# Optimization experiments

Measured on AMD Instinct MI355X. Metric: run time of the kernel, lower is better.

## Reference

```python
import jax, jax.numpy as jnp
import numpy as np

D_MODEL = 1024
NUM_HEADS = 16
D_K = D_MODEL // NUM_HEADS


def setup_inputs() -> dict:
    key = jax.random.key(0)
    ks = jax.random.split(key, 11)
    s = 1.0 / np.sqrt(D_MODEL)
    return {
        "Q": jax.random.normal(ks[0], (2, 2048, D_MODEL), jnp.float32),
        "K": jax.random.normal(ks[1], (2, 2048, D_MODEL), jnp.float32),
        "V": jax.random.normal(ks[2], (2, 2048, D_MODEL), jnp.float32),
        "W_Q": jax.random.uniform(ks[3], (D_MODEL, D_MODEL), jnp.float32, -s, s),
        "b_Q": jax.random.uniform(ks[4], (D_MODEL,), jnp.float32, -s, s),
        "W_K": jax.random.uniform(ks[5], (D_K, D_MODEL), jnp.float32, -s, s),
        "b_K": jax.random.uniform(ks[6], (D_K,), jnp.float32, -s, s),
        "W_V": jax.random.uniform(ks[7], (D_K, D_MODEL), jnp.float32, -s, s),
        "b_V": jax.random.uniform(ks[8], (D_K,), jnp.float32, -s, s),
        "W_O": jax.random.uniform(ks[9], (D_MODEL, D_MODEL), jnp.float32, -s, s),
        "b_O": jax.random.uniform(ks[10], (D_MODEL,), jnp.float32, -s, s),
    }


def reference(Q, K, V, W_Q, b_Q, W_K, b_K, W_V, b_V, W_O, b_O):
    B, S, _ = Q.shape
    # Q projection -> [B, H, S, d_k]
    q = (Q @ W_Q.T + b_Q).reshape(B, S, NUM_HEADS, D_K).transpose(0, 2, 1, 3)
    # shared single-head K/V -> [B, S, d_k] (broadcast across heads)
    k = K @ W_K.T + b_K
    v = V @ W_V.T + b_V
    scale = 1.0 / jnp.sqrt(jnp.asarray(D_K, q.dtype))
    scores = jnp.einsum('bhqd,bkd->bhqk', q, k) * scale  # [B,H,S,S]
    attn = jax.nn.softmax(scores, axis=-1)
    out = jnp.einsum('bhqk,bkd->bhqd', attn, v)  # [B,H,S,d_k]
    out = out.transpose(0, 2, 1, 3).reshape(B, S, D_MODEL)
    return out @ W_O.T + b_O
```

## Files before the change

### kernel.cpp

```cpp
#include <hip/hip_runtime.h>
#include <hip/hip_bf16.h>
#include <math.h>

#define D_MODEL 1024
#define NUM_HEADS 16
#define DK 64
#define BATCH 2
#define SEQ 2048
#define MROWS (BATCH * SEQ)

#define QSCALE (0.125f * 1.4426950408889634f)

typedef __attribute__((ext_vector_type(8))) short bf16x8;
typedef __attribute__((ext_vector_type(4))) float f32x4;

static __device__ __forceinline__ short f2bf(float f) {
    __hip_bfloat16 h = __float2bfloat16(f);
    union { __hip_bfloat16 h; short s; } c; c.h = h; return c.s;
}

static __device__ __forceinline__ unsigned pkbf2(float a, float b) {
    __hip_bfloat162 h = __float22bfloat162_rn(make_float2(a, b));
    union { __hip_bfloat162 h; unsigned u; } c; c.h = h; return c.u;
}

static __device__ __forceinline__ void gload16(const void* g, void* l) {
    __builtin_amdgcn_global_load_lds(
        (const __attribute__((address_space(1))) unsigned int*)g,
        (__attribute__((address_space(3))) unsigned int*)l, 16, 0, 0);
}

__global__ __launch_bounds__(256) void cvt6(
    const float* __restrict__ q, const float* __restrict__ k,
    const float* __restrict__ v, const float* __restrict__ wq,
    const float* __restrict__ wo, const float* __restrict__ wk,
    const float* __restrict__ wv,
    short* __restrict__ qo, short* __restrict__ ko, short* __restrict__ vo,
    short* __restrict__ wqo, short* __restrict__ woo, short* __restrict__ wko,
    short* __restrict__ wvo)
{
    const int NB = (MROWS * D_MODEL) / 8;
    const int NW = (D_MODEL * D_MODEL) / 8;
    const int NS = (DK * D_MODEL) / 8;
    const int total = 3 * NB + 2 * NW + 2 * NS;
    for (int g = blockIdx.x * 256 + threadIdx.x; g < total; g += gridDim.x * 256) {
        const float* s; short* d; int x = g;
        if (x < NB)            { s = q;  d = qo;  }
        else if ((x -= NB) < NB) { s = k;  d = ko;  }
        else if ((x -= NB) < NB) { s = v;  d = vo;  }
        else if ((x -= NB) < NW) { s = wq; d = wqo; }
        else if ((x -= NW) < NW) { s = wo; d = woo; }
        else if ((x -= NW) < NS) { s = wk; d = wko; }
        else                     { x -= NS; s = wv; d = wvo; }
        float4 a = ((const float4*)s)[x * 2];
        float4 b = ((const float4*)s)[x * 2 + 1];
        uint4 hv;
        hv.x = pkbf2(a.x, a.y); hv.y = pkbf2(a.z, a.w);
        hv.z = pkbf2(b.x, b.y); hv.w = pkbf2(b.z, b.w);
        ((uint4*)d)[x] = hv;
    }
}

template<int MODE, int BM, int BN>
__global__ __launch_bounds__(256) void gemm97(
    const short* __restrict__ A, const short* __restrict__ W,
    const float* __restrict__ bias, void* __restrict__ Cp,
    const short* __restrict__ A2, const short* __restrict__ W2,
    const float* __restrict__ bias2, void* __restrict__ Cp2,
    int M, int N, int K, float outmult)
{
    constexpr int MI = BM / 32;
    constexpr int NI = BN / 32;
    constexpr int ACH = BM / 32;
    constexpr int WCH = BN / 32;
    __shared__ short As[BM * 64];
    __shared__ short Ws[BN * 64];

    int sel = 0;
    if (MODE == 2) {
        sel = blockIdx.y;
        if (sel) { A = A2; W = W2; bias = bias2; Cp = Cp2; }
    }
    const int bm = blockIdx.x * BM;
    const int bn = (MODE == 2) ? 0 : blockIdx.y * BN;
    const int tid = threadIdx.x;
    const int l = tid & 63, w = tid >> 6;
    const int lr = l & 15, lg = l >> 4;
    const int wm = (w >> 1) * (BM / 2), wn = (w & 1) * (BN / 2);

    f32x4 acc[MI][NI];
    #pragma unroll
    for (int mi = 0; mi < MI; mi++)
        #pragma unroll
        for (int ni = 0; ni < NI; ni++)
            acc[mi][ni] = (f32x4){0.f, 0.f, 0.f, 0.f};

    const int srow = l >> 3;
    const int scol = (l & 7) * 8;

    for (int k0 = 0; k0 < K; k0 += 64) {
        __syncthreads();
        #pragma unroll
        for (int i = 0; i < ACH; i++) {
            int c = w * ACH + i;
            gload16(A + (size_t)(bm + 8 * c + srow) * K + k0 + scol, As + c * 512);
        }
        #pragma unroll
        for (int i = 0; i < WCH; i++) {
            int c = w * WCH + i;
            gload16(W + (size_t)(bn + 8 * c + srow) * K + k0 + scol, Ws + c * 512);
        }
        __syncthreads();
        #pragma unroll
        for (int ks = 0; ks < 2; ks++) {
            bf16x8 af[MI], bf[NI];
            #pragma unroll
            for (int mi = 0; mi < MI; mi++)
                af[mi] = *(const bf16x8*)&As[(wm + mi * 16 + lr) * 64 + ks * 32 + 8 * lg];
            #pragma unroll
            for (int ni = 0; ni < NI; ni++)
                bf[ni] = *(const bf16x8*)&Ws[(wn + ni * 16 + lr) * 64 + ks * 32 + 8 * lg];
            #pragma unroll
            for (int mi = 0; mi < MI; mi++)
                #pragma unroll
                for (int ni = 0; ni < NI; ni++)
                    acc[mi][ni] = __builtin_amdgcn_mfma_f32_16x16x32_bf16(
                        af[mi], bf[ni], acc[mi][ni], 0, 0, 0);
        }
    }

    #pragma unroll
    for (int ni = 0; ni < NI; ni++) {
        int col = bn + wn + ni * 16 + lr;
        float bv = bias[col];
        #pragma unroll
        for (int mi = 0; mi < MI; mi++) {
            #pragma unroll
            for (int r = 0; r < 4; r++) {
                int row = bm + wm + mi * 16 + lg * 4 + r;
                float val = (acc[mi][ni][r] + bv) * outmult;
                if (MODE == 0) {
                    ((short*)Cp)[(size_t)row * N + col] = f2bf(val);
                } else if (MODE == 1) {
                    ((float*)Cp)[(size_t)row * N + col] = val;
                } else {
                    if (sel == 0) {
                        ((short*)Cp)[(size_t)row * DK + col] = f2bf(val);
                    } else {
                        int bi = row >> 11, si = row & (SEQ - 1);
                        ((short*)Cp)[((size_t)bi * DK + col) * SEQ + si] = f2bf(val);
                    }
                }
            }
        }
    }
}

__global__ __launch_bounds__(256, 3) void mqa_attn_lds(
    const short* __restrict__ qb, const short* __restrict__ kb,
    const short* __restrict__ vt, short* __restrict__ ob)
{
    __shared__ char KsB[2][64 * 128];
    __shared__ char VsB[2][64 * 128];
    __shared__ char Ps[4][32 * 128];
    const int h = blockIdx.y, b = blockIdx.z;
    const int tid = threadIdx.x;
    const int l = tid & 63, w = tid >> 6;
    const int lr = l & 15, lg = l >> 4;
    const int q0 = blockIdx.x * 128 + w * 32;
    char* myPs = Ps[w];

    bf16x8 qf[2][2];
    #pragma unroll
    for (int qt = 0; qt < 2; qt++)
        #pragma unroll
        for (int kk = 0; kk < 2; kk++)
            qf[qt][kk] = *(const bf16x8*)(
                qb + (size_t)(b * SEQ + q0 + qt * 16 + lr) * D_MODEL + h * DK + kk * 32 + 8 * lg);

    int srow[2], scol[2];
    #pragma unroll
    for (int i = 0; i < 2; i++) {
        int s = i * 256 + w * 64 + l;
        srow[i] = s >> 3;
        int cb = (s & 7) * 16;
        scol[i] = (cb ^ ((srow[i] & 7) << 4)) >> 1;
    }

    f32x4 o[4][2];
    #pragma unroll
    for (int dt = 0; dt < 4; dt++)
        #pragma unroll
        for (int qt = 0; qt < 2; qt++)
            o[dt][qt] = (f32x4){0.f, 0.f, 0.f, 0.f};
    float m_i[2] = {-1e30f, -1e30f};
    float l_i[2] = {0.f, 0.f};

    #pragma unroll
    for (int i = 0; i < 2; i++) {
        gload16(kb + (size_t)(b * SEQ + 0 + srow[i]) * DK + scol[i],
                KsB[0] + (i * 256 + w * 64) * 16);
        gload16(vt + (size_t)(b * DK + srow[i]) * SEQ + 0 + scol[i],
                VsB[0] + (i * 256 + w * 64) * 16);
    }

    for (int t = 0; t < SEQ / 64; t++) {
        const int cur = t & 1;
        const int kt = t * 64;
        __syncthreads();
        if (t + 1 < SEQ / 64) {
            const int ktn = kt + 64;
            #pragma unroll
            for (int i = 0; i < 2; i++) {
                gload16(kb + (size_t)(b * SEQ + ktn + srow[i]) * DK + scol[i],
                        KsB[cur ^ 1] + (i * 256 + w * 64) * 16);
                gload16(vt + (size_t)(b * DK + srow[i]) * SEQ + ktn + scol[i],
                        VsB[cur ^ 1] + (i * 256 + w * 64) * 16);
            }
        }
        const char* Kc = KsB[cur];
        const char* Vc = VsB[cur];

        f32x4 s[2][4];
        #pragma unroll
        for (int qt = 0; qt < 2; qt++)
            #pragma unroll
            for (int j = 0; j < 4; j++) s[qt][j] = (f32x4){0.f, 0.f, 0.f, 0.f};
        #pragma unroll
        for (int kk = 0; kk < 2; kk++) {
            bf16x8 kf[4];
            #pragma unroll
            for (int j = 0; j < 4; j++) {
                int row = j * 16 + lr;
                kf[j] = *(const bf16x8*)(Kc + row * 128 + ((kk * 64 + 16 * lg) ^ ((row & 7) << 4)));
            }
            __builtin_amdgcn_s_setprio(1);
            #pragma unroll
            for (int qt = 0; qt < 2; qt++)
                #pragma unroll
                for (int j = 0; j < 4; j++)
                    s[qt][j] = __builtin_amdgcn_mfma_f32_16x16x32_bf16(
                        kf[j], qf[qt][kk], s[qt][j], 0, 0, 0);
            __builtin_amdgcn_s_setprio(0);
        }

        float corr[2]; int resc[2];
        #pragma unroll
        for (int qt = 0; qt < 2; qt++) {
            float mA = fmaxf(fmaxf(s[qt][0][0], s[qt][0][1]), s[qt][0][2]);
            float mB = fmaxf(fmaxf(s[qt][0][3], s[qt][1][0]), s[qt][1][1]);
            float mC = fmaxf(fmaxf(s[qt][1][2], s[qt][1][3]), s[qt][2][0]);
            float mD = fmaxf(fmaxf(s[qt][2][1], s[qt][2][2]), s[qt][2][3]);
            float mE = fmaxf(fmaxf(s[qt][3][0], s[qt][3][1]), s[qt][3][2]);
            float mx = fmaxf(fmaxf(fmaxf(mA, mB), mC),
                             fmaxf(fmaxf(mD, mE), s[qt][3][3]));
            mx = fmaxf(mx, __shfl_xor(mx, 16));
            mx = fmaxf(mx, __shfl_xor(mx, 32));

            resc[qt] = __any(mx > m_i[qt] + 8.0f);
            if (resc[qt]) {
                float mn = fmaxf(m_i[qt], mx);
                corr[qt] = __builtin_amdgcn_exp2f(m_i[qt] - mn);
                m_i[qt] = mn;
            } else {
                corr[qt] = 1.0f;
            }
            const float mnv = m_i[qt];

            float rs = 0.f;
            const int row = qt * 16 + lr;
            char* base = myPs + row * 128;
            const int sw = (row & 7) << 4;
            #pragma unroll
            for (int j = 0; j < 4; j++) {
                float p0 = __builtin_amdgcn_exp2f(s[qt][j][0] - mnv);
                float p1 = __builtin_amdgcn_exp2f(s[qt][j][1] - mnv);
                float p2 = __builtin_amdgcn_exp2f(s[qt][j][2] - mnv);
                float p3 = __builtin_amdgcn_exp2f(s[qt][j][3] - mnv);
                rs += (p0 + p1) + (p2 + p3);
                uint2 pk;
                pk.x = pkbf2(p0, p1);
                pk.y = pkbf2(p2, p3);
                *(uint2*)(base + ((j * 32 + lg * 8) ^ sw)) = pk;
            }
            rs += __shfl_xor(rs, 16);
            rs += __shfl_xor(rs, 32);
            l_i[qt] = l_i[qt] * corr[qt] + rs;
        }
        #pragma unroll
        for (int qt = 0; qt < 2; qt++)
            if (resc[qt]) {
                #pragma unroll
                for (int dt = 0; dt < 4; dt++)
                    o[dt][qt] *= corr[qt];
            }

        #pragma unroll
        for (int kk = 0; kk < 2; kk++) {
            bf16x8 vf[4], pf[2];
            #pragma unroll
            for (int dt = 0; dt < 4; dt++) {
                int row = dt * 16 + lr;
                vf[dt] = *(const bf16x8*)(Vc + row * 128 + ((kk * 64 + 16 * lg) ^ ((row & 7) << 4)));
            }
            #pragma unroll
            for (int qt = 0; qt < 2; qt++) {
                int row = qt * 16 + lr;
                pf[qt] = *(bf16x8*)(myPs + row * 128 + ((kk * 64 + 16 * lg) ^ ((row & 7) << 4)));
            }
            __builtin_amdgcn_s_setprio(1);
            #pragma unroll
            for (int dt = 0; dt < 4; dt++)
                #pragma unroll
                for (int qt = 0; qt < 2; qt++)
                    o[dt][qt] = __builtin_amdgcn_mfma_f32_16x16x32_bf16(
                        vf[dt], pf[qt], o[dt][qt], 0, 0, 0);
            __builtin_amdgcn_s_setprio(0);
        }
    }

    #pragma unroll
    for (int qt = 0; qt < 2; qt++) {
        float inv = 1.0f / l_i[qt];
        size_t grow = (size_t)(b * SEQ + q0 + qt * 16 + lr);
        #pragma unroll
        for (int dt = 0; dt < 4; dt++) {
            uint2 pk;
            pk.x = pkbf2(o[dt][qt][0] * inv, o[dt][qt][1] * inv);
            pk.y = pkbf2(o[dt][qt][2] * inv, o[dt][qt][3] * inv);
            *(uint2*)(ob + grow * D_MODEL + h * DK + dt * 16 + lg * 4) = pk;
        }
    }
}

extern "C" void kernel_launch(void* const* d_in, const int* in_sizes, int n_in,
                              void* d_out, int out_size, void* d_ws, size_t ws_size,
                              hipStream_t stream) {
    const float* Q   = (const float*)d_in[0];
    const float* K   = (const float*)d_in[1];
    const float* V   = (const float*)d_in[2];
    const float* W_Q = (const float*)d_in[3];
    const float* b_Q = (const float*)d_in[4];
    const float* W_K = (const float*)d_in[5];
    const float* b_K = (const float*)d_in[6];
    const float* W_V = (const float*)d_in[7];
    const float* b_V = (const float*)d_in[8];
    const float* W_O = (const float*)d_in[9];
    const float* b_O = (const float*)d_in[10];
    float* out = (float*)d_out;

    short* Qb  = (short*)d_ws;
    short* Kb  = Qb  + (size_t)MROWS * D_MODEL;
    short* Vb  = Kb  + (size_t)MROWS * D_MODEL;
    short* WQb = Vb  + (size_t)MROWS * D_MODEL;
    short* WKb = WQb + (size_t)D_MODEL * D_MODEL;
    short* WVb = WKb + (size_t)DK * D_MODEL;
    short* WOb = WVb + (size_t)DK * D_MODEL;
    short* qb  = WOb + (size_t)D_MODEL * D_MODEL;
    short* kb  = qb  + (size_t)MROWS * D_MODEL;
    short* vt  = kb  + (size_t)MROWS * DK;
    short* aws = vt  + (size_t)MROWS * DK;

    cvt6<<<2048, 256, 0, stream>>>(Q, K, V, W_Q, W_O, W_K, W_V,
                                   Qb, Kb, Vb, WQb, WOb, WKb, WVb);

    gemm97<0, 64, 128><<<dim3(MROWS / 64, D_MODEL / 128), 256, 0, stream>>>(
        Qb, WQb, b_Q, qb, nullptr, nullptr, nullptr, nullptr,
        MROWS, D_MODEL, D_MODEL, QSCALE);
    gemm97<2, 64, 64><<<dim3(MROWS / 64, 2), 256, 0, stream>>>(
        Kb, WKb, b_K, kb, Vb, WVb, b_V, vt, MROWS, DK, D_MODEL, 1.0f);
    mqa_attn_lds<<<dim3(SEQ / 128, NUM_HEADS, BATCH), 256, 0, stream>>>(
        qb, kb, vt, aws);
    gemm97<1, 64, 128><<<dim3(MROWS / 64, D_MODEL / 128), 256, 0, stream>>>(
        aws, WOb, b_O, out, nullptr, nullptr, nullptr, nullptr,
        MROWS, D_MODEL, D_MODEL, 1.0f);
}
```

Measured before the change: 132.5 us.

## Halve attention query tile per wave and defer row-sum reduction

The attention kernel now gives each wave 16 query rows instead of 32, so each block covers 64 queries, the grid doubles, and launch bounds rise to 4 blocks per CU with a smaller P buffer in LDS. The per-row sum reduction across lanes moves out of the KV loop and runs once at the end, and the max shuffle only runs when a rescale is triggered. The aim is more waves and occupancy with fewer cross-lane ops per iteration, at the cost of reloading each K/V tile from global memory for twice as many blocks and lower MFMA reuse per K/V fragment.

```diff
diff --git a/kernel.cpp b/kernel.cpp
--- a/kernel.cpp
+++ b/kernel.cpp
@@ -156,27 +156,25 @@
     }
 }
 
-__global__ __launch_bounds__(256, 3) void mqa_attn_lds(
+__global__ __launch_bounds__(256, 4) void mqa_attn_lds(
     const short* __restrict__ qb, const short* __restrict__ kb,
     const short* __restrict__ vt, short* __restrict__ ob)
 {
     __shared__ char KsB[2][64 * 128];
     __shared__ char VsB[2][64 * 128];
-    __shared__ char Ps[4][32 * 128];
+    __shared__ char Ps[4][16 * 128];
     const int h = blockIdx.y, b = blockIdx.z;
     const int tid = threadIdx.x;
     const int l = tid & 63, w = tid >> 6;
     const int lr = l & 15, lg = l >> 4;
-    const int q0 = blockIdx.x * 128 + w * 32;
+    const int q0 = blockIdx.x * 64 + w * 16;
     char* myPs = Ps[w];
 
-    bf16x8 qf[2][2];
-    #pragma unroll
-    for (int qt = 0; qt < 2; qt++)
-        #pragma unroll
-        for (int kk = 0; kk < 2; kk++)
-            qf[qt][kk] = *(const bf16x8*)(
-                qb + (size_t)(b * SEQ + q0 + qt * 16 + lr) * D_MODEL + h * DK + kk * 32 + 8 * lg);
+    bf16x8 qf[2];
+    #pragma unroll
+    for (int kk = 0; kk < 2; kk++)
+        qf[kk] = *(const bf16x8*)(
+            qb + (size_t)(b * SEQ + q0 + lr) * D_MODEL + h * DK + kk * 32 + 8 * lg);
 
     int srow[2], scol[2];
     #pragma unroll
@@ -187,14 +185,12 @@
         scol[i] = (cb ^ ((srow[i] & 7) << 4)) >> 1;
     }
 
-    f32x4 o[4][2];
+    f32x4 o[4];
     #pragma unroll
     for (int dt = 0; dt < 4; dt++)
-        #pragma unroll
-        for (int qt = 0; qt < 2; qt++)
-            o[dt][qt] = (f32x4){0.f, 0.f, 0.f, 0.f};
-    float m_i[2] = {-1e30f, -1e30f};
-    float l_i[2] = {0.f, 0.f};
+        o[dt] = (f32x4){0.f, 0.f, 0.f, 0.f};
+    float m_i = -1e30f;
+    float l_l = 0.f;
 
     #pragma unroll
     for (int i = 0; i < 2; i++) {
@@ -221,11 +217,9 @@
         const char* Kc = KsB[cur];
         const char* Vc = VsB[cur];
 
-        f32x4 s[2][4];
-        #pragma unroll
-        for (int qt = 0; qt < 2; qt++)
-            #pragma unroll
-            for (int j = 0; j < 4; j++) s[qt][j] = (f32x4){0.f, 0.f, 0.f, 0.f};
+        f32x4 s[4];
+        #pragma unroll
+        for (int j = 0; j < 4; j++) s[j] = (f32x4){0.f, 0.f, 0.f, 0.f};
         #pragma unroll
         for (int kk = 0; kk < 2; kk++) {
             bf16x8 kf[4];
@@ -236,100 +230,81 @@
             }
             __builtin_amdgcn_s_setprio(1);
             #pragma unroll
-            for (int qt = 0; qt < 2; qt++)
+            for (int j = 0; j < 4; j++)
+                s[j] = __builtin_amdgcn_mfma_f32_16x16x32_bf16(
+                    kf[j], qf[kk], s[j], 0, 0, 0);
+            __builtin_amdgcn_s_setprio(0);
+        }
+
+        {
+            float mA = fmaxf(fmaxf(s[0][0], s[0][1]), s[0][2]);
+            float mB = fmaxf(fmaxf(s[0][3], s[1][0]), s[1][1]);
+            float mC = fmaxf(fmaxf(s[1][2], s[1][3]), s[2][0]);
+            float mD = fmaxf(fmaxf(s[2][1], s[2][2]), s[2][3]);
+            float mE = fmaxf(fmaxf(s[3][0], s[3][1]), s[3][2]);
+            float mx = fmaxf(fmaxf(fmaxf(mA, mB), mC),
+                             fmaxf(fmaxf(mD, mE), s[3][3]));
+
+            if (__any(mx > m_i + 8.0f)) {
+                float mxf = fmaxf(mx, __shfl_xor(mx, 16));
+                mxf = fmaxf(mxf, __shfl_xor(mxf, 32));
+                float mn = fmaxf(m_i, mxf);
+                float corr = __builtin_amdgcn_exp2f(m_i - mn);
+                m_i = mn;
+                l_l *= corr;
                 #pragma unroll
-                for (int j = 0; j < 4; j++)
-                    s[qt][j] = __builtin_amdgcn_mfma_f32_16x16x32_bf16(
-                        kf[j], qf[qt][kk], s[qt][j], 0, 0, 0);
-            __builtin_amdgcn_s_setprio(0);
-        }
-
-        float corr[2]; int resc[2];
-        #pragma unroll
-        for (int qt = 0; qt < 2; qt++) {
-            float mA = fmaxf(fmaxf(s[qt][0][0], s[qt][0][1]), s[qt][0][2]);
-            float mB = fmaxf(fmaxf(s[qt][0][3], s[qt][1][0]), s[qt][1][1]);
-            float mC = fmaxf(fmaxf(s[qt][1][2], s[qt][1][3]), s[qt][2][0]);
-            float mD = fmaxf(fmaxf(s[qt][2][1], s[qt][2][2]), s[qt][2][3]);
-            float mE = fmaxf(fmaxf(s[qt][3][0], s[qt][3][1]), s[qt][3][2]);
-            float mx = fmaxf(fmaxf(fmaxf(mA, mB), mC),
-                             fmaxf(fmaxf(mD, mE), s[qt][3][3]));
-            mx = fmaxf(mx, __shfl_xor(mx, 16));
-            mx = fmaxf(mx, __shfl_xor(mx, 32));
-
-            resc[qt] = __any(mx > m_i[qt] + 8.0f);
-            if (resc[qt]) {
-                float mn = fmaxf(m_i[qt], mx);
-                corr[qt] = __builtin_amdgcn_exp2f(m_i[qt] - mn);
-                m_i[qt] = mn;
-            } else {
-                corr[qt] = 1.0f;
-            }
-            const float mnv = m_i[qt];
+                for (int dt = 0; dt < 4; dt++)
+                    o[dt] *= corr;
+            }
+            const float mnv = m_i;
 
             float rs = 0.f;
-            const int row = qt * 16 + lr;
-            char* base = myPs + row * 128;
-            const int sw = (row & 7) << 4;
+            char* base = myPs + lr * 128;
+            const int sw = (lr & 7) << 4;
             #pragma unroll
             for (int j = 0; j < 4; j++) {
-                float p0 = __builtin_amdgcn_exp2f(s[qt][j][0] - mnv);
-                float p1 = __builtin_amdgcn_exp2f(s[qt][j][1] - mnv);
-                float p2 = __builtin_amdgcn_exp2f(s[qt][j][2] - mnv);
-                float p3 = __builtin_amdgcn_exp2f(s[qt][j][3] - mnv);
+                float p0 = __builtin_amdgcn_exp2f(s[j][0] - mnv);
+                float p1 = __builtin_amdgcn_exp2f(s[j][1] - mnv);
+                float p2 = __builtin_amdgcn_exp2f(s[j][2] - mnv);
+                float p3 = __builtin_amdgcn_exp2f(s[j][3] - mnv);
                 rs += (p0 + p1) + (p2 + p3);
                 uint2 pk;
                 pk.x = pkbf2(p0, p1);
                 pk.y = pkbf2(p2, p3);
                 *(uint2*)(base + ((j * 32 + lg * 8) ^ sw)) = pk;
             }
-            rs += __shfl_xor(rs, 16);
-            rs += __shfl_xor(rs, 32);
-            l_i[qt] = l_i[qt] * corr[qt] + rs;
-        }
-        #pragma unroll
-        for (int qt = 0; qt < 2; qt++)
-            if (resc[qt]) {
-                #pragma unroll
-                for (int dt = 0; dt < 4; dt++)
-                    o[dt][qt] *= corr[qt];
-            }
+            l_l += rs;
+        }
 
         #pragma unroll
         for (int kk = 0; kk < 2; kk++) {
-            bf16x8 vf[4], pf[2];
+            bf16x8 vf[4], pf;
             #pragma unroll
             for (int dt = 0; dt < 4; dt++) {
                 int row = dt * 16 + lr;
                 vf[dt] = *(const bf16x8*)(Vc + row * 128 + ((kk * 64 + 16 * lg) ^ ((row & 7) << 4)));
             }
-            #pragma unroll
-            for (int qt = 0; qt < 2; qt++) {
-                int row = qt * 16 + lr;
-                pf[qt] = *(bf16x8*)(myPs + row * 128 + ((kk * 64 + 16 * lg) ^ ((row & 7) << 4)));
-            }
+            pf = *(bf16x8*)(myPs + lr * 128 + ((kk * 64 + 16 * lg) ^ ((lr & 7) << 4)));
             __builtin_amdgcn_s_setprio(1);
             #pragma unroll
             for (int dt = 0; dt < 4; dt++)
-                #pragma unroll
-                for (int qt = 0; qt < 2; qt++)
-                    o[dt][qt] = __builtin_amdgcn_mfma_f32_16x16x32_bf16(
-                        vf[dt], pf[qt], o[dt][qt], 0, 0, 0);
+                o[dt] = __builtin_amdgcn_mfma_f32_16x16x32_bf16(
+                    vf[dt], pf, o[dt], 0, 0, 0);
             __builtin_amdgcn_s_setprio(0);
         }
     }
 
-    #pragma unroll
-    for (int qt = 0; qt < 2; qt++) {
-        float inv = 1.0f / l_i[qt];
-        size_t grow = (size_t)(b * SEQ + q0 + qt * 16 + lr);
-        #pragma unroll
-        for (int dt = 0; dt < 4; dt++) {
-            uint2 pk;
-            pk.x = pkbf2(o[dt][qt][0] * inv, o[dt][qt][1] * inv);
-            pk.y = pkbf2(o[dt][qt][2] * inv, o[dt][qt][3] * inv);
-            *(uint2*)(ob + grow * D_MODEL + h * DK + dt * 16 + lg * 4) = pk;
-        }
+    float lt = l_l;
+    lt += __shfl_xor(lt, 16);
+    lt += __shfl_xor(lt, 32);
+    float inv = 1.0f / lt;
+    size_t grow = (size_t)(b * SEQ + q0 + lr);
+    #pragma unroll
+    for (int dt = 0; dt < 4; dt++) {
+        uint2 pk;
+        pk.x = pkbf2(o[dt][0] * inv, o[dt][1] * inv);
+        pk.y = pkbf2(o[dt][2] * inv, o[dt][3] * inv);
+        *(uint2*)(ob + grow * D_MODEL + h * DK + dt * 16 + lg * 4) = pk;
     }
 }
 
@@ -369,7 +344,7 @@
         MROWS, D_MODEL, D_MODEL, QSCALE);
     gemm97<2, 64, 64><<<dim3(MROWS / 64, 2), 256, 0, stream>>>(
         Kb, WKb, b_K, kb, Vb, WVb, b_V, vt, MROWS, DK, D_MODEL, 1.0f);
-    mqa_attn_lds<<<dim3(SEQ / 128, NUM_HEADS, BATCH), 256, 0, stream>>>(
+    mqa_attn_lds<<<dim3(SEQ / 64, NUM_HEADS, BATCH), 256, 0, stream>>>(
         qb, kb, vt, aws);
     gemm97<1, 64, 128><<<dim3(MROWS / 64, D_MODEL / 128), 256, 0, stream>>>(
         aws, WOb, b_O, out, nullptr, nullptr, nullptr, nullptr,
```

Result: no change. 130.9 us (-1.2%).

## Keep softmax P in registers via permuted V layout; shrink attention blocks to 2 waves

Applied to the files above, without the earlier changes.

The V-transpose GEMM epilogue now writes V with a permuted key order inside each 64-key tile, so the MFMA output layout of the S tile matches the B-operand layout the PV MFMA expects. P can then be packed straight into registers instead of going through a per-wave LDS round-trip. Row sums are kept per lane and reduced only once at the end, and the max shuffle runs only when a rescale is triggered. Attention blocks shrink from 4 to 2 waves (64 queries), which doubles the grid and the K/V tile loads per query row and adds register pressure from the preloaded V fragments.

```diff
diff --git a/kernel.cpp b/kernel.cpp
--- a/kernel.cpp
+++ b/kernel.cpp
@@ -148,7 +148,11 @@
                         ((short*)Cp)[(size_t)row * DK + col] = f2bf(val);
                     } else {
                         int bi = row >> 11, si = row & (SEQ - 1);
-                        ((short*)Cp)[((size_t)bi * DK + col) * SEQ + si] = f2bf(val);
+                        int s6 = si & 63;
+                        int sperm = (si & ~63) | (s6 & 32) |
+                                    (((s6 >> 3) & 1) << 4) | (((s6 >> 2) & 1) << 3) |
+                                    (((s6 >> 4) & 1) << 2) | (s6 & 3);
+                        ((short*)Cp)[((size_t)bi * DK + col) * SEQ + sperm] = f2bf(val);
                     }
                 }
             }
@@ -156,19 +160,17 @@
     }
 }
 
-__global__ __launch_bounds__(256, 3) void mqa_attn_lds(
+__global__ __launch_bounds__(128, 2) void mqa_attn_lds(
     const short* __restrict__ qb, const short* __restrict__ kb,
     const short* __restrict__ vt, short* __restrict__ ob)
 {
     __shared__ char KsB[2][64 * 128];
     __shared__ char VsB[2][64 * 128];
-    __shared__ char Ps[4][32 * 128];
     const int h = blockIdx.y, b = blockIdx.z;
     const int tid = threadIdx.x;
     const int l = tid & 63, w = tid >> 6;
     const int lr = l & 15, lg = l >> 4;
-    const int q0 = blockIdx.x * 128 + w * 32;
-    char* myPs = Ps[w];
+    const int q0 = blockIdx.x * 64 + w * 32;
 
     bf16x8 qf[2][2];
     #pragma unroll
@@ -178,10 +180,10 @@
             qf[qt][kk] = *(const bf16x8*)(
                 qb + (size_t)(b * SEQ + q0 + qt * 16 + lr) * D_MODEL + h * DK + kk * 32 + 8 * lg);
 
-    int srow[2], scol[2];
-    #pragma unroll
-    for (int i = 0; i < 2; i++) {
-        int s = i * 256 + w * 64 + l;
+    int srow[4], scol[4];
+    #pragma unroll
+    for (int i = 0; i < 4; i++) {
+        int s = i * 128 + w * 64 + l;
         srow[i] = s >> 3;
         int cb = (s & 7) * 16;
         scol[i] = (cb ^ ((srow[i] & 7) << 4)) >> 1;
@@ -194,14 +196,14 @@
         for (int qt = 0; qt < 2; qt++)
             o[dt][qt] = (f32x4){0.f, 0.f, 0.f, 0.f};
     float m_i[2] = {-1e30f, -1e30f};
-    float l_i[2] = {0.f, 0.f};
-
-    #pragma unroll
-    for (int i = 0; i < 2; i++) {
+    float l_l[2] = {0.f, 0.f};
+
+    #pragma unroll
+    for (int i = 0; i < 4; i++) {
         gload16(kb + (size_t)(b * SEQ + 0 + srow[i]) * DK + scol[i],
-                KsB[0] + (i * 256 + w * 64) * 16);
+                KsB[0] + (i * 128 + w * 64) * 16);
         gload16(vt + (size_t)(b * DK + srow[i]) * SEQ + 0 + scol[i],
-                VsB[0] + (i * 256 + w * 64) * 16);
+                VsB[0] + (i * 128 + w * 64) * 16);
     }
 
     for (int t = 0; t < SEQ / 64; t++) {
@@ -211,11 +213,11 @@
         if (t + 1 < SEQ / 64) {
             const int ktn = kt + 64;
             #pragma unroll
-            for (int i = 0; i < 2; i++) {
+            for (int i = 0; i < 4; i++) {
                 gload16(kb + (size_t)(b * SEQ + ktn + srow[i]) * DK + scol[i],
-                        KsB[cur ^ 1] + (i * 256 + w * 64) * 16);
+                        KsB[cur ^ 1] + (i * 128 + w * 64) * 16);
                 gload16(vt + (size_t)(b * DK + srow[i]) * SEQ + ktn + scol[i],
-                        VsB[cur ^ 1] + (i * 256 + w * 64) * 16);
+                        VsB[cur ^ 1] + (i * 128 + w * 64) * 16);
             }
         }
         const char* Kc = KsB[cur];
@@ -244,7 +246,16 @@
             __builtin_amdgcn_s_setprio(0);
         }
 
-        float corr[2]; int resc[2];
+        bf16x8 vf[2][4];
+        #pragma unroll
+        for (int kk = 0; kk < 2; kk++)
+            #pragma unroll
+            for (int dt = 0; dt < 4; dt++) {
+                int row = dt * 16 + lr;
+                vf[kk][dt] = *(const bf16x8*)(Vc + row * 128 + ((kk * 64 + 16 * lg) ^ ((row & 7) << 4)));
+            }
+
+        union { unsigned u[4]; bf16x8 v; } pku[2][2];
         #pragma unroll
         for (int qt = 0; qt < 2; qt++) {
             float mA = fmaxf(fmaxf(s[qt][0][0], s[qt][0][1]), s[qt][0][2]);
@@ -254,74 +265,60 @@
             float mE = fmaxf(fmaxf(s[qt][3][0], s[qt][3][1]), s[qt][3][2]);
             float mx = fmaxf(fmaxf(fmaxf(mA, mB), mC),
                              fmaxf(fmaxf(mD, mE), s[qt][3][3]));
-            mx = fmaxf(mx, __shfl_xor(mx, 16));
-            mx = fmaxf(mx, __shfl_xor(mx, 32));
-
-            resc[qt] = __any(mx > m_i[qt] + 8.0f);
-            if (resc[qt]) {
-                float mn = fmaxf(m_i[qt], mx);
-                corr[qt] = __builtin_amdgcn_exp2f(m_i[qt] - mn);
+
+            if (__any(mx > m_i[qt] + 8.0f)) {
+                float mxf = fmaxf(mx, __shfl_xor(mx, 16));
+                mxf = fmaxf(mxf, __shfl_xor(mxf, 32));
+                float mn = fmaxf(m_i[qt], mxf);
+                float corr = __builtin_amdgcn_exp2f(m_i[qt] - mn);
                 m_i[qt] = mn;
-            } else {
-                corr[qt] = 1.0f;
-            }
-            const float mnv = m_i[qt];
-
-            float rs = 0.f;
-            const int row = qt * 16 + lr;
-            char* base = myPs + row * 128;
-            const int sw = (row & 7) << 4;
-            #pragma unroll
-            for (int j = 0; j < 4; j++) {
-                float p0 = __builtin_amdgcn_exp2f(s[qt][j][0] - mnv);
-                float p1 = __builtin_amdgcn_exp2f(s[qt][j][1] - mnv);
-                float p2 = __builtin_amdgcn_exp2f(s[qt][j][2] - mnv);
-                float p3 = __builtin_amdgcn_exp2f(s[qt][j][3] - mnv);
-                rs += (p0 + p1) + (p2 + p3);
-                uint2 pk;
-                pk.x = pkbf2(p0, p1);
-                pk.y = pkbf2(p2, p3);
-                *(uint2*)(base + ((j * 32 + lg * 8) ^ sw)) = pk;
-            }
-            rs += __shfl_xor(rs, 16);
-            rs += __shfl_xor(rs, 32);
-            l_i[qt] = l_i[qt] * corr[qt] + rs;
-        }
-        #pragma unroll
-        for (int qt = 0; qt < 2; qt++)
-            if (resc[qt]) {
+                l_l[qt] *= corr;
                 #pragma unroll
                 for (int dt = 0; dt < 4; dt++)
-                    o[dt][qt] *= corr[qt];
-            }
-
-        #pragma unroll
-        for (int kk = 0; kk < 2; kk++) {
-            bf16x8 vf[4], pf[2];
-            #pragma unroll
-            for (int dt = 0; dt < 4; dt++) {
-                int row = dt * 16 + lr;
-                vf[dt] = *(const bf16x8*)(Vc + row * 128 + ((kk * 64 + 16 * lg) ^ ((row & 7) << 4)));
-            }
-            #pragma unroll
-            for (int qt = 0; qt < 2; qt++) {
-                int row = qt * 16 + lr;
-                pf[qt] = *(bf16x8*)(myPs + row * 128 + ((kk * 64 + 16 * lg) ^ ((row & 7) << 4)));
-            }
-            __builtin_amdgcn_s_setprio(1);
+                    o[dt][qt] *= corr;
+            }
+            const float mnv = m_i[qt];
+
+            float p[4][4];
+            float rs = 0.f;
+            #pragma unroll
+            for (int j = 0; j < 4; j++) {
+                p[j][0] = __builtin_amdgcn_exp2f(s[qt][j][0] - mnv);
+                p[j][1] = __builtin_amdgcn_exp2f(s[qt][j][1] - mnv);
+                p[j][2] = __builtin_amdgcn_exp2f(s[qt][j][2] - mnv);
+                p[j][3] = __builtin_amdgcn_exp2f(s[qt][j][3] - mnv);
+                rs += (p[j][0] + p[j][1]) + (p[j][2] + p[j][3]);
+            }
+            l_l[qt] += rs;
+
+            pku[qt][0].u[0] = pkbf2(p[0][0], p[0][1]);
+            pku[qt][0].u[1] = pkbf2(p[0][2], p[0][3]);
+            pku[qt][0].u[2] = pkbf2(p[1][0], p[1][1]);
+            pku[qt][0].u[3] = pkbf2(p[1][2], p[1][3]);
+            pku[qt][1].u[0] = pkbf2(p[2][0], p[2][1]);
+            pku[qt][1].u[1] = pkbf2(p[2][2], p[2][3]);
+            pku[qt][1].u[2] = pkbf2(p[3][0], p[3][1]);
+            pku[qt][1].u[3] = pkbf2(p[3][2], p[3][3]);
+        }
+
+        __builtin_amdgcn_s_setprio(1);
+        #pragma unroll
+        for (int kk = 0; kk < 2; kk++)
             #pragma unroll
             for (int dt = 0; dt < 4; dt++)
                 #pragma unroll
                 for (int qt = 0; qt < 2; qt++)
                     o[dt][qt] = __builtin_amdgcn_mfma_f32_16x16x32_bf16(
-                        vf[dt], pf[qt], o[dt][qt], 0, 0, 0);
-            __builtin_amdgcn_s_setprio(0);
-        }
+                        vf[kk][dt], pku[qt][kk].v, o[dt][qt], 0, 0, 0);
+        __builtin_amdgcn_s_setprio(0);
     }
 
     #pragma unroll
     for (int qt = 0; qt < 2; qt++) {
-        float inv = 1.0f / l_i[qt];
+        float lt = l_l[qt];
+        lt += __shfl_xor(lt, 16);
+        lt += __shfl_xor(lt, 32);
+        float inv = 1.0f / lt;
         size_t grow = (size_t)(b * SEQ + q0 + qt * 16 + lr);
         #pragma unroll
         for (int dt = 0; dt < 4; dt++) {
@@ -369,7 +366,7 @@
         MROWS, D_MODEL, D_MODEL, QSCALE);
     gemm97<2, 64, 64><<<dim3(MROWS / 64, 2), 256, 0, stream>>>(
         Kb, WKb, b_K, kb, Vb, WVb, b_V, vt, MROWS, DK, D_MODEL, 1.0f);
-    mqa_attn_lds<<<dim3(SEQ / 128, NUM_HEADS, BATCH), 256, 0, stream>>>(
+    mqa_attn_lds<<<dim3(SEQ / 64, NUM_HEADS, BATCH), 128, 0, stream>>>(
         qb, kb, vt, aws);
     gemm97<1, 64, 128><<<dim3(MROWS / 64, D_MODEL / 128), 256, 0, stream>>>(
         aws, WOb, b_O, out, nullptr, nullptr, nullptr, nullptr,
```

After: 131.3 us. No clear change (-0.9%).
